# Kernel tuning notes

Hardware: AMD Instinct MI355X
Metric: run time of the kernel (lower is better)

## Reference

```python
import jax, jax.numpy as jnp
import numpy as np

B, D_IN, D_OUT, E, K, RH = 8192, 1024, 1024, 8, 2, 128

def setup_inputs() -> dict:
    key = jax.random.key(0)
    ks = jax.random.split(key, 7)
    s_in = 1.0 / np.sqrt(D_IN)
    s_rh = 1.0 / np.sqrt(RH)
    return {
        "x": jax.random.normal(ks[0], (B, D_IN), jnp.float32),
        # router: Linear(D_IN, RH) -> tanh -> Linear(RH, E) -> softmax
        "rw1": jax.random.uniform(ks[1], (D_IN, RH), jnp.float32, -s_in, s_in),
        "rb1": jax.random.uniform(ks[2], (RH,), jnp.float32, -s_in, s_in),
        "rw2": jax.random.uniform(ks[3], (RH, E), jnp.float32, -s_rh, s_rh),
        "rb2": jax.random.uniform(ks[4], (E,), jnp.float32, -s_rh, s_rh),
        # experts: E x Linear(D_IN, D_OUT)
        "ew": jax.random.uniform(ks[5], (E, D_IN, D_OUT), jnp.float32, -s_in, s_in),
        "eb": jax.random.uniform(ks[6], (E, D_OUT), jnp.float32, -s_in, s_in),
    }

def reference(x, rw1, rb1, rw2, rb2, ew, eb):
    # router (glu_on=False, gim_input=None): softmax over experts (dim=1)
    h = jnp.tanh(x @ rw1 + rb1)                       # [B, RH]
    probs = jax.nn.softmax(h @ rw2 + rb2, axis=1)     # [B, E]
    ws, ib = jax.lax.top_k(probs, K)                  # [B, K] each
    nws = jax.nn.softmax(ws, axis=1)                  # renormalized top-k weights
    # per-expert GEMM on all tokens (dense-equivalent of masked dispatch)
    y = jnp.einsum("bd,edf->bef", x, ew) + eb         # [B, E, D_OUT]
    # combine weights: scatter nws into [B, E] at selected expert slots
    comb = jnp.zeros((x.shape[0], E), x.dtype).at[
        jnp.arange(x.shape[0])[:, None], ib].add(nws)  # [B, E]
    # weighted scatter-combine (output_type='sum')
    return jnp.einsum("be,bef->bf", comb, y)          # [B, D_OUT]
```

## Files before the change

### kernel.cpp

```cpp
#include <hip/hip_runtime.h>

#define B_TOK   8192
#define D_IN    1024
#define D_OUT   1024
#define NEXP    8
#define RH      128
#define MAXTILES 136
#define MAXSLOTS (MAXTILES*128)

typedef __attribute__((ext_vector_type(8))) short v8s;
typedef __attribute__((ext_vector_type(8))) unsigned short v8u;
typedef __attribute__((ext_vector_type(4))) float v4f;

__device__ __forceinline__ unsigned short f2bf(float f){
  unsigned int u = __float_as_uint(f);
  u += 0x7fffu + ((u >> 16) & 1u);
  return (unsigned short)(u >> 16);
}
__device__ __forceinline__ float bf2f(unsigned short s){
  return __uint_as_float(((unsigned int)s) << 16);
}
__device__ __forceinline__ void gload16(const void* g, void* l){
  __builtin_amdgcn_global_load_lds(
      (const __attribute__((address_space(1))) unsigned int*)g,
      (__attribute__((address_space(3))) unsigned int*)l, 16, 0, 0);
}

__global__ __launch_bounds__(256) void k_cvt_ew(const float* __restrict__ ew,
                                                unsigned short* __restrict__ ewT){
  __shared__ float tile[32][33];
  int tx = threadIdx.x, ty = threadIdx.y;
  int n0 = blockIdx.x*32, k0 = blockIdx.y*32, e = blockIdx.z;
  size_t ebase = (size_t)e << 20;
  #pragma unroll
  for (int i=0;i<4;i++){
    int kl = ty*4+i;
    tile[kl][tx] = ew[ebase + (size_t)(k0+kl)*1024 + n0 + tx];
  }
  __syncthreads();
  #pragma unroll
  for (int i=0;i<4;i++){
    int nl = ty*4+i;
    ewT[ebase + (size_t)(n0+nl)*1024 + (k0 + tx)] = f2bf(tile[tx][nl]);
  }
}

__global__ __launch_bounds__(128) void k_router(
    const float* __restrict__ x,  const float* __restrict__ rw1,
    const float* __restrict__ rb1,const float* __restrict__ rw2,
    const float* __restrict__ rb2,
    unsigned short* __restrict__ xbf,
    int2* __restrict__ tok_ids, float2* __restrict__ tok_w)
{
  __shared__ float xs [64*32];
  __shared__ float ws1[64*128];
  __shared__ float hs [32*129];
  __shared__ float rw2s[RH*NEXP];
  int tid = threadIdx.x;
  int tx = tid & 15, ty = tid >> 4;
  int tok0 = blockIdx.x * 32;
  {
    float4 v0 = *(const float4*)(rw2 + tid*8);
    float4 v1 = *(const float4*)(rw2 + tid*8 + 4);
    *(float4*)(rw2s + tid*8)     = v0;
    *(float4*)(rw2s + tid*8 + 4) = v1;
  }
  float acc[4][8];
  #pragma unroll
  for (int i=0;i<4;i++)
    #pragma unroll
    for (int j=0;j<8;j++) acc[i][j]=0.f;

  for (int k0=0;k0<D_IN;k0+=64){
    {
      int m = tid & 31, cb4 = tid >> 5;
      union { v8u v[2]; unsigned short s[16]; } ub;
      #pragma unroll
      for (int i=0;i<4;i++){
        int chunk = cb4*4 + i;
        float4 v = *(const float4*)(x + (size_t)(tok0+m)*D_IN + k0 + chunk*4);
        xs[(chunk*4+0)*32 + m] = v.x;
        xs[(chunk*4+1)*32 + m] = v.y;
        xs[(chunk*4+2)*32 + m] = v.z;
        xs[(chunk*4+3)*32 + m] = v.w;
        ub.s[i*4+0]=f2bf(v.x); ub.s[i*4+1]=f2bf(v.y);
        ub.s[i*4+2]=f2bf(v.z); ub.s[i*4+3]=f2bf(v.w);
      }
      unsigned short* xo = xbf + (size_t)(tok0+m)*D_IN + k0 + cb4*16;
      *(v8u*)(xo)     = ub.v[0];
      *(v8u*)(xo + 8) = ub.v[1];
    }
    #pragma unroll
    for (int i=0;i<16;i++){
      int idx = tid + 128*i;
      int row = idx >> 5, c4 = (idx & 31)*4;
      *(float4*)(ws1 + row*128 + c4) = *(const float4*)(rw1 + (size_t)(k0+row)*RH + c4);
    }
    __syncthreads();
    #pragma unroll 8
    for (int k=0;k<64;k++){
      float4 a  = *(float4*)(xs  + k*32 + ty*4);
      float4 b0 = *(float4*)(ws1 + k*128 + tx*4);
      float4 b1 = *(float4*)(ws1 + k*128 + 64 + tx*4);
      float av[4] = {a.x,a.y,a.z,a.w};
      float bv[8] = {b0.x,b0.y,b0.z,b0.w,b1.x,b1.y,b1.z,b1.w};
      #pragma unroll
      for (int i=0;i<4;i++)
        #pragma unroll
        for (int j=0;j<8;j++) acc[i][j] += av[i]*bv[j];
    }
    __syncthreads();
  }
  #pragma unroll
  for (int i=0;i<4;i++){
    int m = ty*4+i;
    #pragma unroll
    for (int j=0;j<4;j++){
      hs[m*129 + tx*4 + j]      = tanhf(acc[i][j]   + rb1[tx*4+j]);
      hs[m*129 + 64 + tx*4 + j] = tanhf(acc[i][4+j] + rb1[64+tx*4+j]);
    }
  }
  __syncthreads();
  if (tid < 32){
    int t = tid;
    float l[NEXP];
    #pragma unroll
    for (int e=0;e<NEXP;e++) l[e] = rb2[e];
    for (int r=0;r<RH;r++){
      float h = hs[t*129 + r];
      #pragma unroll
      for (int e=0;e<NEXP;e++) l[e] += h * rw2s[r*8 + e];
    }
    float mx = l[0];
    #pragma unroll
    for (int e=1;e<NEXP;e++) mx = fmaxf(mx, l[e]);
    float p[NEXP], s = 0.f;
    #pragma unroll
    for (int e=0;e<NEXP;e++){ p[e] = expf(l[e]-mx); s += p[e]; }
    float inv = 1.f/s;
    #pragma unroll
    for (int e=0;e<NEXP;e++) p[e] *= inv;
    int bi = 0; float bv = p[0]; int si = -1; float sv = -1.f;
    #pragma unroll
    for (int e=1;e<NEXP;e++){
      if (p[e] > bv){ sv = bv; si = bi; bv = p[e]; bi = e; }
      else if (p[e] > sv){ sv = p[e]; si = e; }
    }
    float e1 = expf(sv - bv);
    float n0 = 1.f/(1.f + e1);
    float n1 = 1.f - n0;
    tok_ids[tok0 + t] = make_int2(bi, si);
    tok_w [tok0 + t] = make_float2(n0, n1);
  }
}

__global__ __launch_bounds__(1024) void k_dispatch(
    const int2* __restrict__ tok_ids, const float2* __restrict__ tok_w,
    int* __restrict__ atok, float* __restrict__ aw,
    int* __restrict__ slotA, int* __restrict__ slotB,
    int2* __restrict__ ttab, int* __restrict__ ntiles)
{
  __shared__ int cnt[NEXP], base[NEXP], cur[NEXP];
  __shared__ int tot;
  int tid = threadIdx.x;
  if (tid < NEXP){ cnt[tid]=0; cur[tid]=0; }
  __syncthreads();
  for (int t=tid; t<B_TOK; t+=1024){
    int2 e = tok_ids[t];
    atomicAdd(&cnt[e.x],1);
    atomicAdd(&cnt[e.y],1);
  }
  __syncthreads();
  if (tid==0){
    int b=0, tt=0;
    for (int e=0;e<NEXP;e++){
      base[e]=b;
      int nt = (cnt[e]+127)>>7;
      for (int i=0;i<nt;i++) ttab[tt++] = make_int2(e, b + i*128);
      b += nt*128;
    }
    tot = b; *ntiles = tt;
  }
  __syncthreads();
  int tt_ = tot;
  for (int s=tid; s<tt_; s+=1024){ atok[s]=0; aw[s]=0.f; }
  __syncthreads();
  for (int t=tid; t<B_TOK; t+=1024){
    int2 e = tok_ids[t]; float2 w = tok_w[t];
    int sA = base[e.x] + atomicAdd(&cur[e.x],1);
    atok[sA]=t; aw[sA]=w.x; slotA[t]=sA;
    int sB = base[e.y] + atomicAdd(&cur[e.y],1);
    atok[sB]=t; aw[sB]=w.y; slotB[t]=sB;
  }
}

__global__ __launch_bounds__(256) void k_gemm(
    const unsigned short* __restrict__ xbf, const unsigned short* __restrict__ ewT,
    const float* __restrict__ eb,
    const int* __restrict__ atok, const float* __restrict__ aw,
    const int2* __restrict__ ttab, const int* __restrict__ ntiles,
    unsigned short* __restrict__ Y)
{
  if ((int)blockIdx.x >= *ntiles) return;
  __shared__ __align__(16) unsigned short As[128*64];
  __shared__ __align__(16) unsigned short Bs[128*64];
  __shared__ int   tokS[128];
  __shared__ float wS[128];
  int tid = threadIdx.x;
  int lane = tid & 63, wid = tid >> 6;
  int2 tt = ttab[blockIdx.x];
  int e = tt.x, slot0 = tt.y;
  int ncol0 = blockIdx.y * 128;
  if (tid < 128){ tokS[tid] = atok[slot0 + tid]; wS[tid] = aw[slot0 + tid]; }
  __syncthreads();
  int rsub = wid*8 + (lane >> 3);
  int cbyte = (lane & 7) * 16;
  const char* xB    = (const char*)xbf;
  const char* eBase = (const char*)ewT + ((size_t)e << 21);
  const char* srcA[4]; const char* srcB[4];
  #pragma unroll
  for (int i=0;i<4;i++){
    srcA[i] = xB    + ((size_t)tokS[i*32 + rsub] << 11) + cbyte;
    srcB[i] = eBase + ((size_t)(ncol0 + i*32 + rsub) << 11) + cbyte;
  }
  v4f zero = {0.f,0.f,0.f,0.f};
  v4f acc[4][4];
  #pragma unroll
  for (int mi=0;mi<4;mi++)
    #pragma unroll
    for (int ni=0;ni<4;ni++) acc[mi][ni] = zero;
  int wr = wid >> 1, wc = wid & 1;
  int fr = lane & 15, fq = lane >> 4;
  unsigned Abase = (unsigned)((wr*64 + fr)*64 + fq*8);
  unsigned Bbase = (unsigned)((wc*64 + fr)*64 + fq*8);

  for (int kt=0; kt<16; ++kt){
    int koff = kt*128;
    #pragma unroll
    for (int i=0;i<4;i++)
      gload16(srcA[i] + koff, (char*)As + (i*32 + wid*8)*128);
    #pragma unroll
    for (int i=0;i<4;i++)
      gload16(srcB[i] + koff, (char*)Bs + (i*32 + wid*8)*128);
    __syncthreads();
    #pragma unroll
    for (int kk=0;kk<2;kk++){
      v8s a[4], b[4];
      #pragma unroll
      for (int mi=0;mi<4;mi++) a[mi] = *(const v8s*)(As + Abase + mi*16*64 + kk*32);
      #pragma unroll
      for (int ni=0;ni<4;ni++) b[ni] = *(const v8s*)(Bs + Bbase + ni*16*64 + kk*32);
      #pragma unroll
      for (int mi=0;mi<4;mi++)
        #pragma unroll
        for (int ni=0;ni<4;ni++)
          acc[mi][ni] = __builtin_amdgcn_mfma_f32_16x16x32_bf16(a[mi], b[ni], acc[mi][ni], 0, 0, 0);
    }
    __syncthreads();
  }
  #pragma unroll
  for (int ni=0;ni<4;ni++){
    int cg = ncol0 + wc*64 + ni*16 + fr;
    float ebv = eb[e*D_OUT + cg];
    #pragma unroll
    for (int mi=0;mi<4;mi++){
      int rb0 = wr*64 + mi*16 + fq*4;
      #pragma unroll
      for (int q=0;q<4;q++){
        int r = rb0 + q;
        float v = wS[r] * (acc[mi][ni][q] + ebv);
        Y[(size_t)(slot0 + r)*D_OUT + cg] = f2bf(v);
      }
    }
  }
}

__global__ __launch_bounds__(256) void k_combine(
    const unsigned short* __restrict__ Y,
    const int* __restrict__ slotA, const int* __restrict__ slotB,
    float* __restrict__ out)
{
  int gid = blockIdx.x*256 + threadIdx.x;
  int t = gid >> 7;
  int c = (gid & 127) << 3;
  v8u a = *(const v8u*)(Y + (size_t)slotA[t]*D_OUT + c);
  v8u b = *(const v8u*)(Y + (size_t)slotB[t]*D_OUT + c);
  float4 o0, o1;
  o0.x = bf2f(a[0]) + bf2f(b[0]);
  o0.y = bf2f(a[1]) + bf2f(b[1]);
  o0.z = bf2f(a[2]) + bf2f(b[2]);
  o0.w = bf2f(a[3]) + bf2f(b[3]);
  o1.x = bf2f(a[4]) + bf2f(b[4]);
  o1.y = bf2f(a[5]) + bf2f(b[5]);
  o1.z = bf2f(a[6]) + bf2f(b[6]);
  o1.w = bf2f(a[7]) + bf2f(b[7]);
  *(float4*)(out + (size_t)t*D_OUT + c)     = o0;
  *(float4*)(out + (size_t)t*D_OUT + c + 4) = o1;
}

extern "C" void kernel_launch(void* const* d_in, const int* in_sizes, int n_in,
                              void* d_out, int out_size, void* d_ws, size_t ws_size,
                              hipStream_t stream)
{
  const float* x   = (const float*)d_in[0];
  const float* rw1 = (const float*)d_in[1];
  const float* rb1 = (const float*)d_in[2];
  const float* rw2 = (const float*)d_in[3];
  const float* rb2 = (const float*)d_in[4];
  const float* ew  = (const float*)d_in[5];
  const float* eb  = (const float*)d_in[6];
  float* out = (float*)d_out;

  char* ws = (char*)d_ws;
  size_t o = 0;
  auto alloc = [&](size_t bytes)->char*{
    char* p = ws + o; o = (o + bytes + 255) & ~(size_t)255; return p;
  };
  unsigned short* xbf = (unsigned short*)alloc((size_t)B_TOK*D_IN*2);
  unsigned short* ewT = (unsigned short*)alloc((size_t)NEXP*D_IN*D_OUT*2);
  unsigned short* Y   = (unsigned short*)alloc((size_t)MAXSLOTS*D_OUT*2);
  int2*   tok_ids = (int2*)  alloc(B_TOK*sizeof(int2));
  float2* tok_w   = (float2*)alloc(B_TOK*sizeof(float2));
  int*    atok    = (int*)   alloc(MAXSLOTS*4);
  float*  aw      = (float*) alloc(MAXSLOTS*4);
  int*    slotA   = (int*)   alloc(B_TOK*4);
  int*    slotB   = (int*)   alloc(B_TOK*4);
  int2*   ttab    = (int2*)  alloc(256*sizeof(int2));
  int*    ntil    = (int*)   alloc(256);
  if (o > ws_size) return;

  k_cvt_ew <<<dim3(32,32,NEXP),  dim3(32,8),  0, stream>>>(ew, ewT);
  k_router <<<dim3(256),         dim3(128),   0, stream>>>(x, rw1, rb1, rw2, rb2, xbf, tok_ids, tok_w);
  k_dispatch<<<dim3(1),          dim3(1024),  0, stream>>>(tok_ids, tok_w, atok, aw, slotA, slotB, ttab, ntil);
  k_gemm   <<<dim3(MAXTILES,8),  dim3(256),   0, stream>>>(xbf, ewT, eb, atok, aw, ttab, ntil, Y);
  k_combine<<<dim3(4096),        dim3(256),   0, stream>>>(Y, slotA, slotB, out);
}
```

Measured before the change: 292.7 us.

## Restructure router kernel to 16-token blocks with 256 threads and parallel logits

The router kernel now processes 16 tokens per block with 256 threads (512 blocks instead of 256 blocks of 128 threads), remapping each thread to 4 tokens by 2 hidden units with padded shared-memory layouts. The second-layer logits are computed by 128 threads in parallel (one token-expert pair each) instead of 32 threads doing all eight experts serially. The aim is more blocks and waves to fill the GPU's compute units and a shorter serial tail in the router. The cost is that each rw1 slab is reloaded by twice as many blocks, and each thread does less FMA work per shared-memory load.

```diff
diff --git a/kernel.cpp b/kernel.cpp
--- a/kernel.cpp
+++ b/kernel.cpp
@@ -10,6 +10,7 @@
 
 typedef __attribute__((ext_vector_type(8))) short v8s;
 typedef __attribute__((ext_vector_type(8))) unsigned short v8u;
+typedef __attribute__((ext_vector_type(4))) unsigned short v4u;
 typedef __attribute__((ext_vector_type(4))) float v4f;
 
 __device__ __forceinline__ unsigned short f2bf(float f){
@@ -45,92 +46,88 @@
   }
 }
 
-__global__ __launch_bounds__(128) void k_router(
+__global__ __launch_bounds__(256) void k_router(
     const float* __restrict__ x,  const float* __restrict__ rw1,
     const float* __restrict__ rb1,const float* __restrict__ rw2,
     const float* __restrict__ rb2,
     unsigned short* __restrict__ xbf,
     int2* __restrict__ tok_ids, float2* __restrict__ tok_w)
 {
-  __shared__ float xs [64*32];
-  __shared__ float ws1[64*128];
-  __shared__ float hs [32*129];
-  __shared__ float rw2s[RH*NEXP];
-  int tid = threadIdx.x;
-  int tx = tid & 15, ty = tid >> 4;
-  int tok0 = blockIdx.x * 32;
+  __shared__ float xs [16*68];
+  __shared__ float ws [64*132];
+  __shared__ float hs [16*132];
+  __shared__ float r2s[RH*NEXP];
+  __shared__ float ls [16*NEXP];
+  int tid  = threadIdx.x;
+  int lane = tid & 63, w = tid >> 6;
+  int g    = lane >> 4;
+  int j    = lane & 15;
+  int rh0  = w*32 + j, rh1 = rh0 + 16;
+  int tok0 = blockIdx.x * 16;
+
   {
-    float4 v0 = *(const float4*)(rw2 + tid*8);
-    float4 v1 = *(const float4*)(rw2 + tid*8 + 4);
-    *(float4*)(rw2s + tid*8)     = v0;
-    *(float4*)(rw2s + tid*8 + 4) = v1;
-  }
-  float acc[4][8];
-  #pragma unroll
-  for (int i=0;i<4;i++)
-    #pragma unroll
-    for (int j=0;j<8;j++) acc[i][j]=0.f;
-
-  for (int k0=0;k0<D_IN;k0+=64){
+    *(float4*)(r2s + tid*4) = *(const float4*)(rw2 + tid*4);
+  }
+  float acc[4][2];
+  #pragma unroll
+  for (int i=0;i<4;i++){ acc[i][0]=0.f; acc[i][1]=0.f; }
+
+  for (int slab=0; slab<16; ++slab){
+    int k0 = slab*64;
     {
-      int m = tid & 31, cb4 = tid >> 5;
-      union { v8u v[2]; unsigned short s[16]; } ub;
-      #pragma unroll
-      for (int i=0;i<4;i++){
-        int chunk = cb4*4 + i;
-        float4 v = *(const float4*)(x + (size_t)(tok0+m)*D_IN + k0 + chunk*4);
-        xs[(chunk*4+0)*32 + m] = v.x;
-        xs[(chunk*4+1)*32 + m] = v.y;
-        xs[(chunk*4+2)*32 + m] = v.z;
-        xs[(chunk*4+3)*32 + m] = v.w;
-        ub.s[i*4+0]=f2bf(v.x); ub.s[i*4+1]=f2bf(v.y);
-        ub.s[i*4+2]=f2bf(v.z); ub.s[i*4+3]=f2bf(v.w);
+      int t = tid >> 4, c4 = tid & 15;
+      float4 v = *(const float4*)(x + (size_t)(tok0+t)*D_IN + k0 + c4*4);
+      *(float4*)(xs + t*68 + c4*4) = v;
+      v4u ub = { f2bf(v.x), f2bf(v.y), f2bf(v.z), f2bf(v.w) };
+      *(v4u*)(xbf + (size_t)(tok0+t)*D_IN + k0 + c4*4) = ub;
+    }
+    #pragma unroll
+    for (int i=0;i<8;i++){
+      int idx = tid + 256*i;
+      int r = idx >> 5, c4 = (idx & 31)*4;
+      *(float4*)(ws + r*132 + c4) = *(const float4*)(rw1 + (size_t)(k0+r)*RH + c4);
+    }
+    __syncthreads();
+    #pragma unroll 4
+    for (int k=0;k<64;k+=4){
+      v4f xv[4];
+      #pragma unroll
+      for (int i=0;i<4;i++) xv[i] = *(v4f*)(xs + (g*4+i)*68 + k);
+      #pragma unroll
+      for (int kk=0;kk<4;kk++){
+        float w0 = ws[(k+kk)*132 + rh0];
+        float w1 = ws[(k+kk)*132 + rh1];
+        #pragma unroll
+        for (int i=0;i<4;i++){
+          acc[i][0] += xv[i][kk] * w0;
+          acc[i][1] += xv[i][kk] * w1;
+        }
       }
-      unsigned short* xo = xbf + (size_t)(tok0+m)*D_IN + k0 + cb4*16;
-      *(v8u*)(xo)     = ub.v[0];
-      *(v8u*)(xo + 8) = ub.v[1];
-    }
-    #pragma unroll
-    for (int i=0;i<16;i++){
-      int idx = tid + 128*i;
-      int row = idx >> 5, c4 = (idx & 31)*4;
-      *(float4*)(ws1 + row*128 + c4) = *(const float4*)(rw1 + (size_t)(k0+row)*RH + c4);
     }
     __syncthreads();
-    #pragma unroll 8
-    for (int k=0;k<64;k++){
-      float4 a  = *(float4*)(xs  + k*32 + ty*4);
-      float4 b0 = *(float4*)(ws1 + k*128 + tx*4);
-      float4 b1 = *(float4*)(ws1 + k*128 + 64 + tx*4);
-      float av[4] = {a.x,a.y,a.z,a.w};
-      float bv[8] = {b0.x,b0.y,b0.z,b0.w,b1.x,b1.y,b1.z,b1.w};
-      #pragma unroll
-      for (int i=0;i<4;i++)
-        #pragma unroll
-        for (int j=0;j<8;j++) acc[i][j] += av[i]*bv[j];
-    }
-    __syncthreads();
-  }
-  #pragma unroll
-  for (int i=0;i<4;i++){
-    int m = ty*4+i;
-    #pragma unroll
-    for (int j=0;j<4;j++){
-      hs[m*129 + tx*4 + j]      = tanhf(acc[i][j]   + rb1[tx*4+j]);
-      hs[m*129 + 64 + tx*4 + j] = tanhf(acc[i][4+j] + rb1[64+tx*4+j]);
-    }
-  }
-  __syncthreads();
-  if (tid < 32){
+  }
+  {
+    float b0 = rb1[rh0], b1 = rb1[rh1];
+    #pragma unroll
+    for (int i=0;i<4;i++){
+      hs[(g*4+i)*132 + rh0] = tanhf(acc[i][0] + b0);
+      hs[(g*4+i)*132 + rh1] = tanhf(acc[i][1] + b1);
+    }
+  }
+  __syncthreads();
+  if (tid < 16*NEXP){
+    int t = tid >> 3, e = tid & 7;
+    float l = rb2[e];
+    #pragma unroll 4
+    for (int r=0;r<RH;r++) l += hs[t*132 + r] * r2s[r*8 + e];
+    ls[t*8 + e] = l;
+  }
+  __syncthreads();
+  if (tid < 16){
     int t = tid;
     float l[NEXP];
     #pragma unroll
-    for (int e=0;e<NEXP;e++) l[e] = rb2[e];
-    for (int r=0;r<RH;r++){
-      float h = hs[t*129 + r];
-      #pragma unroll
-      for (int e=0;e<NEXP;e++) l[e] += h * rw2s[r*8 + e];
-    }
+    for (int e=0;e<NEXP;e++) l[e] = ls[t*8 + e];
     float mx = l[0];
     #pragma unroll
     for (int e=1;e<NEXP;e++) mx = fmaxf(mx, l[e]);
@@ -330,7 +327,7 @@
   if (o > ws_size) return;
 
   k_cvt_ew <<<dim3(32,32,NEXP),  dim3(32,8),  0, stream>>>(ew, ewT);
-  k_router <<<dim3(256),         dim3(128),   0, stream>>>(x, rw1, rb1, rw2, rb2, xbf, tok_ids, tok_w);
+  k_router <<<dim3(512),         dim3(256),   0, stream>>>(x, rw1, rb1, rw2, rb2, xbf, tok_ids, tok_w);
   k_dispatch<<<dim3(1),          dim3(1024),  0, stream>>>(tok_ids, tok_w, atok, aw, slotA, slotB, ttab, ntil);
   k_gemm   <<<dim3(MAXTILES,8),  dim3(256),   0, stream>>>(xbf, ewT, eb, atok, aw, ttab, ntil, Y);
   k_combine<<<dim3(4096),        dim3(256),   0, stream>>>(Y, slotA, slotB, out);
```

New measurement: 282.7 us. -3.4%, faster.
